# Kernel optimization log

Measured on AMD Instinct MI355X. Metric: run time of the kernel, lower is better.

The kernel has to match this reference:

```python
import jax, jax.numpy as jnp
import numpy as np

ITER_ROUTING = 3
EPS = 1e-9


def setup_inputs() -> dict:
    key = jax.random.key(0)
    k1, = jax.random.split(key, 1)
    B, N, C, D = 16, 16384, 10, 16
    votes = jax.random.normal(k1, (B, N, C, D), dtype=jnp.float32)
    activation = jnp.ones((B, N, 1), dtype=jnp.float32)
    beta_v = jnp.zeros((C, D), dtype=jnp.float32)
    beta_a = jnp.zeros((C,), dtype=jnp.float32)
    return {"votes": votes, "activation": activation, "beta_v": beta_v, "beta_a": beta_a}


def reference(votes, activation, beta_v, beta_a):
    # EM routing per DigitCaps.em_routing; returns miu (= v) of shape [B,1,C,D]
    B, N, C, D = votes.shape
    miu = None
    sigma_sq = None
    act_out = None
    for iters in range(ITER_ROUTING):
        if iters == 0:
            r = jnp.full((B, N, C), 1.0 / C, dtype=votes.dtype)
        else:
            # log p(vote | gaussian_j), per channel: [B,N,C,D]
            log_p = -0.5 * jnp.log(sigma_sq) - jnp.square(votes - miu) / (2.0 * sigma_sq)
            # numerical shift as in original (max over capsule+channel dims, minus log 10)
            log_p = log_p - (jnp.max(log_p, axis=(2, 3), keepdims=True) - jnp.log(10.0))
            p_c = jnp.exp(jnp.sum(log_p, axis=3))                 # [B,N,C]
            ap = p_c * act_out.reshape(B, 1, C)                    # [B,N,C]
            r = ap / (jnp.sum(ap, axis=2, keepdims=True) + EPS)
        r = r * activation                                         # [B,N,C] (activation broadcasts [B,N,1])
        r = r / (jnp.sum(r, axis=2, keepdims=True) + EPS)
        r_sum = jnp.sum(r, axis=1, keepdims=True)                  # [B,1,C]
        r1 = (r / (r_sum + EPS))[..., None]                        # [B,N,C,1]
        miu = jnp.sum(votes * r1, axis=1, keepdims=True)           # [B,1,C,D]
        sigma_sq = jnp.sum(jnp.square(votes - miu) * r1, axis=1, keepdims=True) + EPS
        if iters == ITER_ROUTING - 1:
            r_sum_c = r_sum.reshape(B, C, 1)
            cost_h = (beta_v + 0.5 * jnp.log(sigma_sq.reshape(B, C, D))) * r_sum_c
            act_out = jax.nn.softmax(0.01 * (beta_a - jnp.sum(cost_h, axis=2)), axis=-1)
        else:
            act_out = jax.nn.softmax(r_sum, axis=-1)               # softmax over C
    return miu
```

## Files before the change

### kernel.cpp

```cpp
#include <hip/hip_runtime.h>
#include <math.h>


namespace {
constexpr int BB = 16, NN = 16384, CC = 10, DD = 16;
constexpr float EPSF = 1e-9f;
constexpr int CHUNKS = 64;
constexpr int ROWS = NN / CHUNKS;
constexpr int ACC_SZ = BB * CC * DD * 2 + BB * CC;
constexpr int RV_OFF = 0;
constexpr int RV2_OFF = BB * CC * DD;
constexpr int RS_OFF = 2 * BB * CC * DD;
constexpr int PMIU = 0;
constexpr int PI2S = BB * CC * DD;
constexpr int PASUM = 2 * BB * CC * DD;
constexpr int PACT = 2 * BB * CC * DD + BB * CC;
constexpr int PAR_SZ = 2 * BB * CC * DD + 2 * BB * CC;
}

__global__ void zero_acc(float* acc, int n) {
  int i = blockIdx.x * blockDim.x + threadIdx.x;
  if (i < n) acc[i] = 0.0f;
}

template <int IT>
__global__ __launch_bounds__(256) void pass_k(const float* __restrict__ votes,
                                              const float* __restrict__ activ,
                                              const float* __restrict__ par,
                                              float* __restrict__ acc, int nbuf) {
  const int b = blockIdx.x / CHUNKS;
  const int chunk = blockIdx.x - b * CHUNKS;
  const int tid = threadIdx.x;
  const int wave = tid >> 6;
  const int lane = tid & 63;
  const int rg = lane & 31;
  const int c = rg >> 1;
  const int half = rg & 1;
  const int cc = c < CC ? c : CC - 1;
  const bool on = c < CC;
  const int rslot = (lane >> 5) + wave * 2;

  __shared__ float L_rv[4][20][8];
  __shared__ float L_rw[4][20][8];
  __shared__ float L_rs[4][CC];

  float4 mi0 = make_float4(0.f, 0.f, 0.f, 0.f), mi1 = mi0;
  float4 is0 = mi0, is1 = mi0;
  float Asum = 0.f, actc = 0.f;
  if (IT != 0) {
    const float* pb = par + (b * CC + cc) * DD + half * 8;
    mi0 = *(const float4*)(pb + PMIU);
    mi1 = *(const float4*)(pb + PMIU + 4);
    is0 = *(const float4*)(pb + PI2S);
    is1 = *(const float4*)(pb + PI2S + 4);
    Asum = par[PASUM + b * CC + cc];
    actc = par[PACT + b * CC + cc];
  }

  float4 rv0 = make_float4(0.f, 0.f, 0.f, 0.f), rv1 = rv0;
  float4 rw0 = rv0, rw1 = rv0;
  float ar = 0.f;

  const int n0 = chunk * ROWS;
  const size_t rowoff = (size_t)cc * DD + half * 8;

  for (int k = rslot; k < ROWS; k += 8) {
    const int n = n0 + k;
    const float* vb = votes + (size_t)(b * NN + n) * (CC * DD) + rowoff;
    const float4 q0 = *(const float4*)vb;
    const float4 q1 = *(const float4*)(vb + 4);
    const float a = activ[b * NN + n];
    float r;
    if (IT == 0) {
      r = (a * (1.0f / CC)) / (a + EPSF);
      ar += r;
    } else {
      float dx, s8 = 0.f;
      dx = q0.x - mi0.x; s8 += dx * dx * is0.x;
      dx = q0.y - mi0.y; s8 += dx * dx * is0.y;
      dx = q0.z - mi0.z; s8 += dx * dx * is0.z;
      dx = q0.w - mi0.w; s8 += dx * dx * is0.w;
      dx = q1.x - mi1.x; s8 += dx * dx * is1.x;
      dx = q1.y - mi1.y; s8 += dx * dx * is1.y;
      dx = q1.z - mi1.z; s8 += dx * dx * is1.z;
      dx = q1.w - mi1.w; s8 += dx * dx * is1.w;
      const float S = Asum - (s8 + __shfl_xor(s8, 1));
      float M = on ? S : -1e30f;
      M = fmaxf(M, __shfl_xor(M, 2));
      M = fmaxf(M, __shfl_xor(M, 4));
      M = fmaxf(M, __shfl_xor(M, 8));
      M = fmaxf(M, __shfl_xor(M, 16));
      const float te = on ? __expf(S - M) * actc : 0.f;
      float sap = te;
      sap += __shfl_xor(sap, 2);
      sap += __shfl_xor(sap, 4);
      sap += __shfl_xor(sap, 8);
      sap += __shfl_xor(sap, 16);
      const float inv = 1.0f / (sap + EPSF);
      const float sr = a * sap * inv;
      r = (te * inv * a) / (sr + EPSF);
      ar += r;
    }
    const float t0x = r * q0.x, t0y = r * q0.y, t0z = r * q0.z, t0w = r * q0.w;
    const float t1x = r * q1.x, t1y = r * q1.y, t1z = r * q1.z, t1w = r * q1.w;
    rv0.x += t0x; rv0.y += t0y; rv0.z += t0z; rv0.w += t0w;
    rv1.x += t1x; rv1.y += t1y; rv1.z += t1z; rv1.w += t1w;
    if (IT <= 1) {
      rw0.x += t0x * q0.x; rw0.y += t0y * q0.y; rw0.z += t0z * q0.z; rw0.w += t0w * q0.w;
      rw1.x += t1x * q1.x; rw1.y += t1y * q1.y; rw1.z += t1z * q1.z; rw1.w += t1w * q1.w;
    }
  }

  rv0.x += __shfl_down(rv0.x, 32); rv0.y += __shfl_down(rv0.y, 32);
  rv0.z += __shfl_down(rv0.z, 32); rv0.w += __shfl_down(rv0.w, 32);
  rv1.x += __shfl_down(rv1.x, 32); rv1.y += __shfl_down(rv1.y, 32);
  rv1.z += __shfl_down(rv1.z, 32); rv1.w += __shfl_down(rv1.w, 32);
  if (IT <= 1) {
    rw0.x += __shfl_down(rw0.x, 32); rw0.y += __shfl_down(rw0.y, 32);
    rw0.z += __shfl_down(rw0.z, 32); rw0.w += __shfl_down(rw0.w, 32);
    rw1.x += __shfl_down(rw1.x, 32); rw1.y += __shfl_down(rw1.y, 32);
    rw1.z += __shfl_down(rw1.z, 32); rw1.w += __shfl_down(rw1.w, 32);
  }
  ar += __shfl_down(ar, 32);

  if (lane < 32 && on) {
    *(float4*)&L_rv[wave][rg][0] = rv0;
    *(float4*)&L_rv[wave][rg][4] = rv1;
    if (IT <= 1) {
      *(float4*)&L_rw[wave][rg][0] = rw0;
      *(float4*)&L_rw[wave][rg][4] = rw1;
    }
    if (half == 0) L_rs[wave][c] = ar;
  }
  __syncthreads();

  float* accr = acc + (size_t)(chunk % nbuf) * ACC_SZ;
  if (tid < CC * DD) {
    const int tc = tid >> 4, td = tid & 15;
    const int rgi = tc * 2 + (td >> 3), dd = td & 7;
    const float s = L_rv[0][rgi][dd] + L_rv[1][rgi][dd] +
                    L_rv[2][rgi][dd] + L_rv[3][rgi][dd];
    atomicAdd(&accr[RV_OFF + (b * CC + tc) * DD + td], s);
    if (IT <= 1) {
      const float s2 = L_rw[0][rgi][dd] + L_rw[1][rgi][dd] +
                       L_rw[2][rgi][dd] + L_rw[3][rgi][dd];
      atomicAdd(&accr[RV2_OFF + (b * CC + tc) * DD + td], s2);
    }
  } else if (tid < CC * DD + CC) {
    const int tc = tid - CC * DD;
    const float s = L_rs[0][tc] + L_rs[1][tc] + L_rs[2][tc] + L_rs[3][tc];
    atomicAdd(&accr[RS_OFF + b * CC + tc], s);
  }
}

template <int MODE>
__global__ void finalize_k(const float* __restrict__ acc, float* __restrict__ par_out,
                           float* __restrict__ out, int nbuf) {
  const int idx = blockIdx.x * blockDim.x + threadIdx.x;
  if (idx < BB * CC * DD) {
    const int bc = idx / DD;
    float rs = 0.f, rv = 0.f;
    for (int k = 0; k < nbuf; ++k) {
      rs += acc[k * ACC_SZ + RS_OFF + bc];
      rv += acc[k * ACC_SZ + RV_OFF + idx];
    }
    const float den = rs + EPSF;
    const float miu = rv / den;
    if (MODE == 1) {
      out[idx] = miu;
    } else {
      float rv2 = 0.f;
      for (int k = 0; k < nbuf; ++k) rv2 += acc[k * ACC_SZ + RV2_OFF + idx];
      const float Sf = rs / den;
      const float sig = rv2 / den - miu * miu * (2.0f - Sf) + EPSF;
      par_out[PMIU + idx] = miu;
      par_out[PI2S + idx] = 0.5f / sig;
      if ((idx & (DD - 1)) == 0) {
        float prod = 1.0f;
        for (int d = 0; d < DD; ++d) {
          float rvd = 0.f, rv2d = 0.f;
          for (int k = 0; k < nbuf; ++k) {
            rvd += acc[k * ACC_SZ + RV_OFF + bc * DD + d];
            rv2d += acc[k * ACC_SZ + RV2_OFF + bc * DD + d];
          }
          const float m2 = rvd / den;
          const float s2 = rv2d / den - m2 * m2 * (2.0f - Sf) + EPSF;
          prod *= s2;
        }
        par_out[PASUM + bc] = -0.5f * logf(prod);
      }
    }
  }
  if (MODE == 0 && blockIdx.x == 0 && threadIdx.x < BB) {
    const int b = threadIdx.x;
    float rsv[CC];
    for (int i = 0; i < CC; ++i) {
      float s = 0.f;
      for (int k = 0; k < nbuf; ++k) s += acc[k * ACC_SZ + RS_OFF + b * CC + i];
      rsv[i] = s;
    }
    float m = -1e30f;
    for (int i = 0; i < CC; ++i) m = fmaxf(m, rsv[i]);
    float ss = 0.f;
    for (int i = 0; i < CC; ++i) ss += __expf(rsv[i] - m);
    for (int i = 0; i < CC; ++i) par_out[PACT + b * CC + i] = __expf(rsv[i] - m) / ss;
  }
}

extern "C" void kernel_launch(void* const* d_in, const int* in_sizes, int n_in,
                              void* d_out, int out_size, void* d_ws, size_t ws_size,
                              hipStream_t stream) {
  const float* votes = (const float*)d_in[0];
  const float* activ = (const float*)d_in[1];
  float* ws = (float*)d_ws;
  float* out = (float*)d_out;

  const int nbuf =
      (ws_size >= (size_t)(4 * ACC_SZ + 2 * PAR_SZ) * sizeof(float)) ? 4 : 3;

  float* acc = ws;
  float* par0 = ws + (size_t)nbuf * ACC_SZ;
  float* par1 = par0 + PAR_SZ;

  const int accN = nbuf * ACC_SZ;
  const dim3 gz((accN + 255) / 256), bz(256);
  const dim3 gp(BB * CHUNKS), bp(256);
  const dim3 gf((BB * CC * DD + 255) / 256), bf(256);

  zero_acc<<<gz, bz, 0, stream>>>(acc, accN);
  pass_k<0><<<gp, bp, 0, stream>>>(votes, activ, nullptr, acc, nbuf);
  finalize_k<0><<<gf, bf, 0, stream>>>(acc, par0, nullptr, nbuf);

  zero_acc<<<gz, bz, 0, stream>>>(acc, accN);
  pass_k<1><<<gp, bp, 0, stream>>>(votes, activ, par0, acc, nbuf);
  finalize_k<0><<<gf, bf, 0, stream>>>(acc, par1, nullptr, nbuf);

  zero_acc<<<gz, bz, 0, stream>>>(acc, accN);
  pass_k<2><<<gp, bp, 0, stream>>>(votes, activ, par1, acc, nbuf);
  finalize_k<1><<<gf, bf, 0, stream>>>(acc, nullptr, out, nbuf);
}
```

Measured before the change: 131.4 us.

## Map one lane per capsule row and fold accumulator zeroing into finalize

Each lane now handles a full 16-wide capsule row (four float4 loads) instead of half a row, so 16 lanes cover a vote row and each wave processes four rows per step. This removes the cross-half shuffle and lowers the lane waste from 12 of 32 to 6 of 16 per row group. Separately, the accumulators are double-buffered and the next pass's buffer is zeroed inside finalize, which drops two zero_acc launches. The trade-off is higher register pressure, with launch_bounds(256,4) added to cap it, plus an extra shuffle stage in the fold.

```diff
diff --git a/kernel.cpp b/kernel.cpp
--- a/kernel.cpp
+++ b/kernel.cpp
@@ -24,78 +24,89 @@
 }
 
 template <int IT>
-__global__ __launch_bounds__(256) void pass_k(const float* __restrict__ votes,
-                                              const float* __restrict__ activ,
-                                              const float* __restrict__ par,
-                                              float* __restrict__ acc, int nbuf) {
+__global__ __launch_bounds__(256, 4) void pass_k(const float* __restrict__ votes,
+                                                 const float* __restrict__ activ,
+                                                 const float* __restrict__ par,
+                                                 float* __restrict__ acc, int nbuf) {
   const int b = blockIdx.x / CHUNKS;
   const int chunk = blockIdx.x - b * CHUNKS;
   const int tid = threadIdx.x;
   const int wave = tid >> 6;
   const int lane = tid & 63;
-  const int rg = lane & 31;
-  const int c = rg >> 1;
-  const int half = rg & 1;
-  const int cc = c < CC ? c : CC - 1;
-  const bool on = c < CC;
-  const int rslot = (lane >> 5) + wave * 2;
-
-  __shared__ float L_rv[4][20][8];
-  __shared__ float L_rw[4][20][8];
+  const int cslot = lane & 15;
+  const int cc = cslot < CC ? cslot : CC - 1;
+  const bool on = cslot < CC;
+  const int rslot = wave * 4 + (lane >> 4);
+
+  __shared__ float L_rv[4][CC][DD];
+  __shared__ float L_rw[4][CC][DD];
   __shared__ float L_rs[4][CC];
 
-  float4 mi0 = make_float4(0.f, 0.f, 0.f, 0.f), mi1 = mi0;
-  float4 is0 = mi0, is1 = mi0;
+  float4 mi0 = make_float4(0.f, 0.f, 0.f, 0.f), mi1 = mi0, mi2 = mi0, mi3 = mi0;
+  float4 is0 = mi0, is1 = mi0, is2 = mi0, is3 = mi0;
   float Asum = 0.f, actc = 0.f;
   if (IT != 0) {
-    const float* pb = par + (b * CC + cc) * DD + half * 8;
+    const float* pb = par + (b * CC + cc) * DD;
     mi0 = *(const float4*)(pb + PMIU);
     mi1 = *(const float4*)(pb + PMIU + 4);
+    mi2 = *(const float4*)(pb + PMIU + 8);
+    mi3 = *(const float4*)(pb + PMIU + 12);
     is0 = *(const float4*)(pb + PI2S);
     is1 = *(const float4*)(pb + PI2S + 4);
+    is2 = *(const float4*)(pb + PI2S + 8);
+    is3 = *(const float4*)(pb + PI2S + 12);
     Asum = par[PASUM + b * CC + cc];
     actc = par[PACT + b * CC + cc];
   }
 
-  float4 rv0 = make_float4(0.f, 0.f, 0.f, 0.f), rv1 = rv0;
-  float4 rw0 = rv0, rw1 = rv0;
+  float4 rv0 = make_float4(0.f, 0.f, 0.f, 0.f), rv1 = rv0, rv2 = rv0, rv3 = rv0;
+  float4 rw0 = rv0, rw1 = rv0, rw2 = rv0, rw3 = rv0;
   float ar = 0.f;
 
   const int n0 = chunk * ROWS;
-  const size_t rowoff = (size_t)cc * DD + half * 8;
-
-  for (int k = rslot; k < ROWS; k += 8) {
+
+  for (int k = rslot; k < ROWS; k += 16) {
     const int n = n0 + k;
-    const float* vb = votes + (size_t)(b * NN + n) * (CC * DD) + rowoff;
+    const float* vb = votes + (size_t)(b * NN + n) * (CC * DD) + cc * DD;
     const float4 q0 = *(const float4*)vb;
     const float4 q1 = *(const float4*)(vb + 4);
+    const float4 q2 = *(const float4*)(vb + 8);
+    const float4 q3 = *(const float4*)(vb + 12);
     const float a = activ[b * NN + n];
     float r;
     if (IT == 0) {
       r = (a * (1.0f / CC)) / (a + EPSF);
       ar += r;
     } else {
-      float dx, s8 = 0.f;
-      dx = q0.x - mi0.x; s8 += dx * dx * is0.x;
-      dx = q0.y - mi0.y; s8 += dx * dx * is0.y;
-      dx = q0.z - mi0.z; s8 += dx * dx * is0.z;
-      dx = q0.w - mi0.w; s8 += dx * dx * is0.w;
-      dx = q1.x - mi1.x; s8 += dx * dx * is1.x;
-      dx = q1.y - mi1.y; s8 += dx * dx * is1.y;
-      dx = q1.z - mi1.z; s8 += dx * dx * is1.z;
-      dx = q1.w - mi1.w; s8 += dx * dx * is1.w;
-      const float S = Asum - (s8 + __shfl_xor(s8, 1));
+      float dx, s = 0.f;
+      dx = q0.x - mi0.x; s += dx * dx * is0.x;
+      dx = q0.y - mi0.y; s += dx * dx * is0.y;
+      dx = q0.z - mi0.z; s += dx * dx * is0.z;
+      dx = q0.w - mi0.w; s += dx * dx * is0.w;
+      dx = q1.x - mi1.x; s += dx * dx * is1.x;
+      dx = q1.y - mi1.y; s += dx * dx * is1.y;
+      dx = q1.z - mi1.z; s += dx * dx * is1.z;
+      dx = q1.w - mi1.w; s += dx * dx * is1.w;
+      dx = q2.x - mi2.x; s += dx * dx * is2.x;
+      dx = q2.y - mi2.y; s += dx * dx * is2.y;
+      dx = q2.z - mi2.z; s += dx * dx * is2.z;
+      dx = q2.w - mi2.w; s += dx * dx * is2.w;
+      dx = q3.x - mi3.x; s += dx * dx * is3.x;
+      dx = q3.y - mi3.y; s += dx * dx * is3.y;
+      dx = q3.z - mi3.z; s += dx * dx * is3.z;
+      dx = q3.w - mi3.w; s += dx * dx * is3.w;
+      const float S = Asum - s;
       float M = on ? S : -1e30f;
+      M = fmaxf(M, __shfl_xor(M, 1));
       M = fmaxf(M, __shfl_xor(M, 2));
       M = fmaxf(M, __shfl_xor(M, 4));
       M = fmaxf(M, __shfl_xor(M, 8));
-      M = fmaxf(M, __shfl_xor(M, 16));
       const float te = on ? __expf(S - M) * actc : 0.f;
       float sap = te;
+      sap += __shfl_xor(sap, 1);
       sap += __shfl_xor(sap, 2);
       sap += __shfl_xor(sap, 4);
       sap += __shfl_xor(sap, 8);
-      sap += __shfl_xor(sap, 16);
       const float inv = 1.0f / (sap + EPSF);
       const float sr = a * sap * inv;
       r = (te * inv * a) / (sr + EPSF);
@@ -103,47 +114,58 @@
     }
     const float t0x = r * q0.x, t0y = r * q0.y, t0z = r * q0.z, t0w = r * q0.w;
     const float t1x = r * q1.x, t1y = r * q1.y, t1z = r * q1.z, t1w = r * q1.w;
+    const float t2x = r * q2.x, t2y = r * q2.y, t2z = r * q2.z, t2w = r * q2.w;
+    const float t3x = r * q3.x, t3y = r * q3.y, t3z = r * q3.z, t3w = r * q3.w;
     rv0.x += t0x; rv0.y += t0y; rv0.z += t0z; rv0.w += t0w;
     rv1.x += t1x; rv1.y += t1y; rv1.z += t1z; rv1.w += t1w;
+    rv2.x += t2x; rv2.y += t2y; rv2.z += t2z; rv2.w += t2w;
+    rv3.x += t3x; rv3.y += t3y; rv3.z += t3z; rv3.w += t3w;
     if (IT <= 1) {
       rw0.x += t0x * q0.x; rw0.y += t0y * q0.y; rw0.z += t0z * q0.z; rw0.w += t0w * q0.w;
       rw1.x += t1x * q1.x; rw1.y += t1y * q1.y; rw1.z += t1z * q1.z; rw1.w += t1w * q1.w;
-    }
-  }
-
-  rv0.x += __shfl_down(rv0.x, 32); rv0.y += __shfl_down(rv0.y, 32);
-  rv0.z += __shfl_down(rv0.z, 32); rv0.w += __shfl_down(rv0.w, 32);
-  rv1.x += __shfl_down(rv1.x, 32); rv1.y += __shfl_down(rv1.y, 32);
-  rv1.z += __shfl_down(rv1.z, 32); rv1.w += __shfl_down(rv1.w, 32);
+      rw2.x += t2x * q2.x; rw2.y += t2y * q2.y; rw2.z += t2z * q2.z; rw2.w += t2w * q2.w;
+      rw3.x += t3x * q3.x; rw3.y += t3y * q3.y; rw3.z += t3z * q3.z; rw3.w += t3w * q3.w;
+    }
+  }
+
+#define FOLD(v) v += __shfl_down(v, 32); v += __shfl_down(v, 16)
+  FOLD(rv0.x); FOLD(rv0.y); FOLD(rv0.z); FOLD(rv0.w);
+  FOLD(rv1.x); FOLD(rv1.y); FOLD(rv1.z); FOLD(rv1.w);
+  FOLD(rv2.x); FOLD(rv2.y); FOLD(rv2.z); FOLD(rv2.w);
+  FOLD(rv3.x); FOLD(rv3.y); FOLD(rv3.z); FOLD(rv3.w);
   if (IT <= 1) {
-    rw0.x += __shfl_down(rw0.x, 32); rw0.y += __shfl_down(rw0.y, 32);
-    rw0.z += __shfl_down(rw0.z, 32); rw0.w += __shfl_down(rw0.w, 32);
-    rw1.x += __shfl_down(rw1.x, 32); rw1.y += __shfl_down(rw1.y, 32);
-    rw1.z += __shfl_down(rw1.z, 32); rw1.w += __shfl_down(rw1.w, 32);
-  }
-  ar += __shfl_down(ar, 32);
-
-  if (lane < 32 && on) {
-    *(float4*)&L_rv[wave][rg][0] = rv0;
-    *(float4*)&L_rv[wave][rg][4] = rv1;
+    FOLD(rw0.x); FOLD(rw0.y); FOLD(rw0.z); FOLD(rw0.w);
+    FOLD(rw1.x); FOLD(rw1.y); FOLD(rw1.z); FOLD(rw1.w);
+    FOLD(rw2.x); FOLD(rw2.y); FOLD(rw2.z); FOLD(rw2.w);
+    FOLD(rw3.x); FOLD(rw3.y); FOLD(rw3.z); FOLD(rw3.w);
+  }
+  FOLD(ar);
+#undef FOLD
+
+  if (lane < CC) {
+    *(float4*)&L_rv[wave][lane][0] = rv0;
+    *(float4*)&L_rv[wave][lane][4] = rv1;
+    *(float4*)&L_rv[wave][lane][8] = rv2;
+    *(float4*)&L_rv[wave][lane][12] = rv3;
     if (IT <= 1) {
-      *(float4*)&L_rw[wave][rg][0] = rw0;
-      *(float4*)&L_rw[wave][rg][4] = rw1;
-    }
-    if (half == 0) L_rs[wave][c] = ar;
+      *(float4*)&L_rw[wave][lane][0] = rw0;
+      *(float4*)&L_rw[wave][lane][4] = rw1;
+      *(float4*)&L_rw[wave][lane][8] = rw2;
+      *(float4*)&L_rw[wave][lane][12] = rw3;
+    }
+    L_rs[wave][lane] = ar;
   }
   __syncthreads();
 
   float* accr = acc + (size_t)(chunk % nbuf) * ACC_SZ;
   if (tid < CC * DD) {
     const int tc = tid >> 4, td = tid & 15;
-    const int rgi = tc * 2 + (td >> 3), dd = td & 7;
-    const float s = L_rv[0][rgi][dd] + L_rv[1][rgi][dd] +
-                    L_rv[2][rgi][dd] + L_rv[3][rgi][dd];
+    const float s = L_rv[0][tc][td] + L_rv[1][tc][td] +
+                    L_rv[2][tc][td] + L_rv[3][tc][td];
     atomicAdd(&accr[RV_OFF + (b * CC + tc) * DD + td], s);
     if (IT <= 1) {
-      const float s2 = L_rw[0][rgi][dd] + L_rw[1][rgi][dd] +
-                       L_rw[2][rgi][dd] + L_rw[3][rgi][dd];
+      const float s2 = L_rw[0][tc][td] + L_rw[1][tc][td] +
+                       L_rw[2][tc][td] + L_rw[3][tc][td];
       atomicAdd(&accr[RV2_OFF + (b * CC + tc) * DD + td], s2);
     }
   } else if (tid < CC * DD + CC) {
@@ -155,7 +177,8 @@
 
 template <int MODE>
 __global__ void finalize_k(const float* __restrict__ acc, float* __restrict__ par_out,
-                           float* __restrict__ out, int nbuf) {
+                           float* __restrict__ out, int nbuf,
+                           float* __restrict__ zbuf, int zn) {
   const int idx = blockIdx.x * blockDim.x + threadIdx.x;
   if (idx < BB * CC * DD) {
     const int bc = idx / DD;
@@ -205,6 +228,10 @@
     for (int i = 0; i < CC; ++i) ss += __expf(rsv[i] - m);
     for (int i = 0; i < CC; ++i) par_out[PACT + b * CC + i] = __expf(rsv[i] - m) / ss;
   }
+  if (MODE == 0) {
+    const int stride = gridDim.x * blockDim.x;
+    for (int i = idx; i < zn; i += stride) zbuf[i] = 0.0f;
+  }
 }
 
 extern "C" void kernel_launch(void* const* d_in, const int* in_sizes, int n_in,
@@ -215,27 +242,24 @@
   float* ws = (float*)d_ws;
   float* out = (float*)d_out;
 
-  const int nbuf =
-      (ws_size >= (size_t)(4 * ACC_SZ + 2 * PAR_SZ) * sizeof(float)) ? 4 : 3;
-
-  float* acc = ws;
-  float* par0 = ws + (size_t)nbuf * ACC_SZ;
+  int nbuf = 1;
+  if (ws_size >= (size_t)(2 * 4 * ACC_SZ + 2 * PAR_SZ) * sizeof(float)) nbuf = 4;
+  else if (ws_size >= (size_t)(2 * 2 * ACC_SZ + 2 * PAR_SZ) * sizeof(float)) nbuf = 2;
+
+  const int accN = nbuf * ACC_SZ;
+  float* accA = ws;
+  float* accB = ws + accN;
+  float* par0 = ws + 2 * accN;
   float* par1 = par0 + PAR_SZ;
 
-  const int accN = nbuf * ACC_SZ;
-  const dim3 gz((accN + 255) / 256), bz(256);
   const dim3 gp(BB * CHUNKS), bp(256);
   const dim3 gf((BB * CC * DD + 255) / 256), bf(256);
 
-  zero_acc<<<gz, bz, 0, stream>>>(acc, accN);
-  pass_k<0><<<gp, bp, 0, stream>>>(votes, activ, nullptr, acc, nbuf);
-  finalize_k<0><<<gf, bf, 0, stream>>>(acc, par0, nullptr, nbuf);
-
-  zero_acc<<<gz, bz, 0, stream>>>(acc, accN);
-  pass_k<1><<<gp, bp, 0, stream>>>(votes, activ, par0, acc, nbuf);
-  finalize_k<0><<<gf, bf, 0, stream>>>(acc, par1, nullptr, nbuf);
-
-  zero_acc<<<gz, bz, 0, stream>>>(acc, accN);
-  pass_k<2><<<gp, bp, 0, stream>>>(votes, activ, par1, acc, nbuf);
-  finalize_k<1><<<gf, bf, 0, stream>>>(acc, nullptr, out, nbuf);
-}
+  zero_acc<<<dim3((accN + 255) / 256), dim3(256), 0, stream>>>(accA, accN);
+  pass_k<0><<<gp, bp, 0, stream>>>(votes, activ, nullptr, accA, nbuf);
+  finalize_k<0><<<gf, bf, 0, stream>>>(accA, par0, nullptr, nbuf, accB, accN);
+  pass_k<1><<<gp, bp, 0, stream>>>(votes, activ, par0, accB, nbuf);
+  finalize_k<0><<<gf, bf, 0, stream>>>(accB, par1, nullptr, nbuf, accA, accN);
+  pass_k<2><<<gp, bp, 0, stream>>>(votes, activ, par1, accA, nbuf);
+  finalize_k<1><<<gf, bf, 0, stream>>>(accA, nullptr, out, nbuf, nullptr, 0);
+}
```

New measurement: 126.1 us. 1.04x faster.
